# Kernel tuning notes

Measured on AMD Instinct MI355X. Metric: run time of the kernel, lower is better.

## Reference

```python
import jax, jax.numpy as jnp
import numpy as np

N, D, E_LOCAL, E_GLOBAL = 50000, 128, 500000, 600000


def gcn_conv(x, W, b, src, dst, w, n):
    """PyG GCNConv with add_self_loops=True, symmetric normalization.

    deg[i] = sum of incoming edge weights at i + 1 (self-loop weight 1)
    norm_e = deg^-1/2[src] * w_e * deg^-1/2[dst]
    out[i] = sum_e norm_e * (xW)[src_e]  +  deg^-1[i] * (xW)[i]  + b
    """
    xw = x @ W  # [n, out]
    deg = jax.ops.segment_sum(w, dst, num_segments=n) + 1.0
    dinv = jnp.where(deg > 0, jax.lax.rsqrt(deg), 0.0)
    norm = dinv[src] * w * dinv[dst]  # [E]
    agg = jax.ops.segment_sum(norm[:, None] * xw[src], dst, num_segments=n)
    self_loop = (dinv * dinv)[:, None] * xw
    return agg + self_loop + b


def setup_inputs() -> dict:
    key = jax.random.key(0)
    ks = jax.random.split(key, 10)
    activity = jax.random.normal(ks[0], (N, D), dtype=jnp.float32)
    learning = jax.random.normal(ks[1], (N, D), dtype=jnp.float32)
    edge_index = jax.random.randint(ks[2], (2, E_LOCAL), 0, N, dtype=jnp.int32)
    edge_weight = jax.random.uniform(ks[3], (E_LOCAL,), dtype=jnp.float32)
    global_edge_index = jax.random.randint(ks[4], (2, E_GLOBAL), 0, N, dtype=jnp.int32)
    global_edge_weight = jax.random.uniform(ks[5], (E_GLOBAL,), dtype=jnp.float32)
    s = 1.0 / np.sqrt(D)
    W_local = jax.random.uniform(ks[6], (D, D), jnp.float32, -s, s)
    b_local = jnp.zeros((D,), jnp.float32)
    W_global = jax.random.uniform(ks[7], (D, D), jnp.float32, -s, s)
    b_global = jnp.zeros((D,), jnp.float32)
    return {
        "activity": activity, "learning": learning,
        "edge_index": edge_index, "edge_weight": edge_weight,
        "global_edge_index": global_edge_index, "global_edge_weight": global_edge_weight,
        "W_local": W_local, "b_local": b_local,
        "W_global": W_global, "b_global": b_global,
    }


def reference(activity, learning, edge_index, edge_weight,
              global_edge_index, global_edge_weight,
              W_local, b_local, W_global, b_global):
    n = activity.shape[0]
    xa = activity + learning
    # Note: GCNConv1 branches in the original are dead code (outputs overwritten);
    # only GCNConv2 (local and global) affect the output.
    xl = gcn_conv(xa, W_local, b_local, edge_index[0], edge_index[1], edge_weight, n)
    xg = gcn_conv(xa, W_global, b_global, global_edge_index[0], global_edge_index[1], global_edge_weight, n)
    wei = jax.nn.sigmoid(xl + xg)
    return 2.0 * activity * wei + 2.0 * learning * (1.0 - wei)
```

## Files before the change

### kernel.cpp

```cpp
#include <hip/hip_runtime.h>

#define DFEAT 128

typedef __attribute__((ext_vector_type(8))) short short8;
typedef __attribute__((ext_vector_type(4))) float float4v;

__device__ __forceinline__ float bf2f(unsigned int h) {
    union { unsigned int u; float f; } v; v.u = h << 16; return v.f;
}
__device__ __forceinline__ unsigned short f2bf(float f) {
    union { float f; unsigned int u; } v; v.f = f;
    unsigned int u = v.u;
    unsigned int lsb = (u >> 16) & 1u;
    u += 0x7fffu + lsb;
    return (unsigned short)(u >> 16);
}

__global__ __launch_bounds__(256) void zprep_kernel(
    const float* __restrict__ Wl, const float* __restrict__ Wg,
    unsigned short* __restrict__ WT,
    unsigned long long* __restrict__ dc, int n2)
{
    if (blockIdx.x < 128) {
        int idx = blockIdx.x * 256 + threadIdx.x;
        int m = idx >> 14, rem = idx & 16383;
        int k = rem >> 7, c = rem & 127;
        const float* W = m ? Wg : Wl;
        WT[m * 16384 + c * 128 + k] = f2bf(W[k * 128 + c]);
        return;
    }
    int i = (blockIdx.x - 128) * 256 + threadIdx.x;
    if (i < n2) dc[i] = 0ULL;
}

__global__ __launch_bounds__(256) void gemm_hist_kernel(
    const float* __restrict__ A, const float* __restrict__ L,
    const unsigned short* __restrict__ WT,
    unsigned short* __restrict__ xwl, unsigned short* __restrict__ xwg,
    const int* __restrict__ dstL, const float* __restrict__ wL,
    const int* __restrict__ dstG, const float* __restrict__ wG,
    unsigned long long* __restrict__ dc, unsigned short* __restrict__ lp16,
    int El, int Eg, int n, int GB)
{
    if (blockIdx.x >= GB) {
        int e = (blockIdx.x - GB) * 256 + threadIdx.x;
        if (e < El) {
            int t = dstL[e];
            unsigned long long add = (1ULL << 48) | (unsigned long long)(wL[e] * 0x1p40f);
            unsigned long long old = atomicAdd(&dc[t], add);
            lp16[e] = (unsigned short)(old >> 48);
        } else if (e < El + Eg) {
            int e2 = e - El;
            int t = dstG[e2];
            unsigned long long add = (1ULL << 48) | (unsigned long long)(wG[e2] * 0x1p40f);
            unsigned long long old = atomicAdd(&dc[n + t], add);
            lp16[e] = (unsigned short)(old >> 48);
        }
        return;
    }
    const int tid  = threadIdx.x;
    const int wid  = tid >> 6;
    const int lane = tid & 63;
    const int quad = lane >> 4;
    const int cl   = lane & 15;

    int rowa = blockIdx.x * 64 + wid * 16 + cl;
    if (rowa > n - 1) rowa = n - 1;

    const float* Ar = A + (size_t)rowa * DFEAT;
    const float* Lr = L + (size_t)rowa * DFEAT;

    short8 a[4];
    #pragma unroll
    for (int kk = 0; kk < 4; ++kk) {
        const int kb = kk * 32 + quad * 8;
        float4 a0 = *(const float4*)&Ar[kb];
        float4 a1 = *(const float4*)&Ar[kb + 4];
        float4 l0 = *(const float4*)&Lr[kb];
        float4 l1 = *(const float4*)&Lr[kb + 4];
        union { short8 v; unsigned short u[8]; } s;
        s.u[0] = f2bf(a0.x + l0.x); s.u[1] = f2bf(a0.y + l0.y);
        s.u[2] = f2bf(a0.z + l0.z); s.u[3] = f2bf(a0.w + l0.w);
        s.u[4] = f2bf(a1.x + l1.x); s.u[5] = f2bf(a1.y + l1.y);
        s.u[6] = f2bf(a1.z + l1.z); s.u[7] = f2bf(a1.w + l1.w);
        a[kk] = s.v;
    }

    const int rbase = blockIdx.x * 64 + wid * 16 + quad * 4;
    const char* wtb = (const char*)WT + quad * 16;

    #pragma unroll
    for (int m = 0; m < 2; ++m) {
        unsigned short* out = m ? xwg : xwl;
        #pragma unroll
        for (int t = 0; t < 8; ++t) {
            const int col = t * 16 + cl;
            const char* bp = wtb + m * 32768 + col * 256;
            float4v acc = {0.f, 0.f, 0.f, 0.f};
            #pragma unroll
            for (int kk = 0; kk < 4; ++kk) {
                short8 b = *(const short8*)(bp + kk * 64);
                acc = __builtin_amdgcn_mfma_f32_16x16x32_bf16(a[kk], b, acc, 0, 0, 0);
            }
            #pragma unroll
            for (int r = 0; r < 4; ++r) {
                int ro = rbase + r;
                if (ro < n) out[(size_t)ro * DFEAT + col] = f2bf(acc[r]);
            }
        }
    }
}

__global__ __launch_bounds__(256) void scan1_kernel(const unsigned long long* __restrict__ dc,
                                                    int* __restrict__ ptr,
                                                    int* __restrict__ bsum,
                                                    float* __restrict__ dinv, int n)
{
    __shared__ int tmp[256];
    int i = blockIdx.x * 256 + threadIdx.x;
    int v = 0;
    if (i < n) {
        unsigned long long d = dc[i];
        v = (int)(d >> 48);
        dinv[i] = rsqrtf((float)(d & ((1ULL << 48) - 1)) * 0x1p-40f + 1.0f);
    }
    tmp[threadIdx.x] = v;
    __syncthreads();
    for (int off = 1; off < 256; off <<= 1) {
        int t = (threadIdx.x >= off) ? tmp[threadIdx.x - off] : 0;
        __syncthreads();
        tmp[threadIdx.x] += t;
        __syncthreads();
    }
    if (i < n) ptr[i] = tmp[threadIdx.x] - v;
    if (threadIdx.x == 255) bsum[blockIdx.x] = tmp[255];
}

__global__ __launch_bounds__(512) void scan2_kernel(int* __restrict__ bsum, int nb)
{
    __shared__ int tmp[512];
    int i = threadIdx.x;
    int v = (i < nb) ? bsum[i] : 0;
    tmp[i] = v;
    __syncthreads();
    for (int off = 1; off < 512; off <<= 1) {
        int t = (i >= off) ? tmp[i - off] : 0;
        __syncthreads();
        tmp[i] += t;
        __syncthreads();
    }
    if (i < nb) bsum[i] = tmp[i] - v;
}

__global__ __launch_bounds__(256) void edata_write_kernel(
    const int* __restrict__ srcL, const int* __restrict__ dstL, const float* __restrict__ wL,
    const int* __restrict__ srcG, const int* __restrict__ dstG, const float* __restrict__ wG,
    const float* __restrict__ dinv, const int* __restrict__ ptr, const int* __restrict__ bsum,
    const unsigned short* __restrict__ lp16, int2* __restrict__ edata,
    int El, int Eg, int n)
{
    int e = blockIdx.x * 256 + threadIdx.x;
    if (e < El) {
        int s = srcL[e], t = dstL[e];
        float norm = dinv[s] * wL[e] * dinv[t];
        int pos = ptr[t] + bsum[t >> 8] + lp16[e];
        edata[pos] = make_int2(__float_as_int(norm), s);
    } else if (e < El + Eg) {
        int e2 = e - El;
        int s = srcG[e2], t = dstG[e2];
        float norm = dinv[n + s] * wG[e2] * dinv[n + t];
        int tt = n + t;
        int pos = ptr[tt] + bsum[tt >> 8] + lp16[e];
        edata[pos] = make_int2(__float_as_int(norm), s);
    }
}

__global__ __launch_bounds__(256) void gather_kernel(
    const unsigned short* __restrict__ xwl, const unsigned short* __restrict__ xwg,
    const int* __restrict__ ptr, const int* __restrict__ bsum, const int2* __restrict__ edata,
    const float* __restrict__ dinv,
    const float* __restrict__ A, const float* __restrict__ Lr,
    const float* __restrict__ bl, const float* __restrict__ bg,
    float* __restrict__ out, int n, int E)
{
    const int lane = threadIdx.x & 63;
    const int node = blockIdx.x * 4 + (threadIdx.x >> 6);
    if (node >= n) return;
    const int i0l = ptr[node] + bsum[node >> 8];
    const int i1l = ptr[node + 1] + bsum[(node + 1) >> 8];
    const int i0g = ptr[n + node] + bsum[(n + node) >> 8];
    const int i1g = (node == n - 1) ? E : ptr[n + node + 1] + bsum[(n + node + 1) >> 8];
    float dl = dinv[node];     dl *= dl;
    float dg = dinv[n + node]; dg *= dg;
    const int fo = 2 * lane;
    const size_t base = (size_t)node * DFEAT + fo;

    unsigned int psl = *(const unsigned int*)&xwl[base];
    unsigned int psg = *(const unsigned int*)&xwg[base];
    float acc0 = dl * bf2f(psl & 0xffffu) + dg * bf2f(psg & 0xffffu);
    float acc1 = dl * bf2f(psl >> 16)     + dg * bf2f(psg >> 16);

    for (int b0 = i0l; b0 < i1l; b0 += 64) {
        int idx = b0 + lane;
        int2 ed = edata[idx < i1l ? idx : (i1l - 1)];
        float nmv = __int_as_float(ed.x);
        int   sv  = ed.y;
        int mcnt = i1l - b0; if (mcnt > 64) mcnt = 64;
        #pragma unroll 4
        for (int jj = 0; jj < mcnt; ++jj) {
            float nm = __shfl(nmv, jj);
            int   s  = __shfl(sv, jj);
            unsigned int pk = *(const unsigned int*)&xwl[(size_t)s * DFEAT + fo];
            acc0 += nm * bf2f(pk & 0xffffu);
            acc1 += nm * bf2f(pk >> 16);
        }
    }
    for (int b0 = i0g; b0 < i1g; b0 += 64) {
        int idx = b0 + lane;
        int2 ed = edata[idx < i1g ? idx : (i1g - 1)];
        float nmv = __int_as_float(ed.x);
        int   sv  = ed.y;
        int mcnt = i1g - b0; if (mcnt > 64) mcnt = 64;
        #pragma unroll 4
        for (int jj = 0; jj < mcnt; ++jj) {
            float nm = __shfl(nmv, jj);
            int   s  = __shfl(sv, jj);
            unsigned int pk = *(const unsigned int*)&xwg[(size_t)s * DFEAT + fo];
            acc0 += nm * bf2f(pk & 0xffffu);
            acc1 += nm * bf2f(pk >> 16);
        }
    }

    float2 b1 = *(const float2*)&bl[fo];
    float2 b2 = *(const float2*)&bg[fo];
    float2 a2 = *(const float2*)&A[base];
    float2 l2 = *(const float2*)&Lr[base];
    float v0 = acc0 + b1.x + b2.x;
    float v1 = acc1 + b1.y + b2.y;
    float w0 = 1.0f / (1.0f + __expf(-v0));
    float w1 = 1.0f / (1.0f + __expf(-v1));
    float o0 = 2.0f * (a2.x * w0 + l2.x * (1.0f - w0));
    float o1 = 2.0f * (a2.y * w1 + l2.y * (1.0f - w1));
    *(float2*)&out[base] = make_float2(o0, o1);
}

extern "C" void kernel_launch(void* const* d_in, const int* in_sizes, int n_in,
                              void* d_out, int out_size, void* d_ws, size_t ws_size,
                              hipStream_t stream)
{
    const float* activity = (const float*)d_in[0];
    const float* learning = (const float*)d_in[1];
    const int*   ei  = (const int*)d_in[2];
    const float* ew  = (const float*)d_in[3];
    const int*   gei = (const int*)d_in[4];
    const float* gew = (const float*)d_in[5];
    const float* Wl  = (const float*)d_in[6];
    const float* bl  = (const float*)d_in[7];
    const float* Wg  = (const float*)d_in[8];
    const float* bg  = (const float*)d_in[9];

    const int n  = in_sizes[0] / DFEAT;
    const int El = in_sizes[3];
    const int Eg = in_sizes[5];
    const int n2 = 2 * n;
    const int E  = El + Eg;

    char* ws = (char*)d_ws;
    const size_t xwBytes = (size_t)n * DFEAT * 2;
    unsigned short* xwl = (unsigned short*)ws;
    unsigned short* xwg = (unsigned short*)(ws + xwBytes);
    unsigned long long* dc = (unsigned long long*)(ws + 2 * xwBytes);
    float* dinv = (float*)(ws + 2 * xwBytes + (size_t)n2 * 8);
    int*   ptr  = (int*)(ws + 2 * xwBytes + (size_t)n2 * 12);
    int*   bsum = (int*)(ws + 2 * xwBytes + (size_t)n2 * 16);
    unsigned short* WT = (unsigned short*)(ws + 2 * xwBytes + (size_t)n2 * 16 + 2048);
    int2* edata = (int2*)(ws + 2 * xwBytes + (size_t)n2 * 16 + 2048 + 65536);
    unsigned short* lp16 = (unsigned short*)(ws + 2 * xwBytes + (size_t)n2 * 16 + 2048 + 65536
                                             + (size_t)E * 8);

    const int scanBlocks = (n2 + 255) / 256;
    const int GB = (n + 63) / 64;
    const int HB = (E + 255) / 256;

    zprep_kernel<<<dim3(128 + scanBlocks), dim3(256), 0, stream>>>(Wl, Wg, WT, dc, n2);

    gemm_hist_kernel<<<dim3(GB + HB), dim3(256), 0, stream>>>(
        activity, learning, WT, xwl, xwg,
        ei + El, ew, gei + Eg, gew, dc, lp16, El, Eg, n, GB);

    scan1_kernel<<<dim3(scanBlocks), dim3(256), 0, stream>>>(dc, ptr, bsum, dinv, n2);
    scan2_kernel<<<dim3(1), dim3(512), 0, stream>>>(bsum, scanBlocks);

    edata_write_kernel<<<dim3(HB), dim3(256), 0, stream>>>(
        ei, ei + El, ew, gei, gei + Eg, gew, dinv, ptr, bsum, lp16, edata, El, Eg, n);

    gather_kernel<<<dim3((n + 3) / 4), dim3(256), 0, stream>>>(
        xwl, xwg, ptr, bsum, edata, dinv, activity, learning, bl, bg, (float*)d_out, n, E);
}
```

Before: 277.3 us.

## Split wavefront into four edge groups with 16-byte feature loads in gather

```diff
diff --git a/kernel.cpp b/kernel.cpp
--- a/kernel.cpp
+++ b/kernel.cpp
@@ -14,6 +14,12 @@
     unsigned int lsb = (u >> 16) & 1u;
     u += 0x7fffu + lsb;
     return (unsigned short)(u >> 16);
+}
+__device__ __forceinline__ float blo(unsigned int u) {
+    union { unsigned int x; float f; } v; v.x = u << 16; return v.f;
+}
+__device__ __forceinline__ float bhi(unsigned int u) {
+    union { unsigned int x; float f; } v; v.x = u & 0xffff0000u; return v.f;
 }
 
 __global__ __launch_bounds__(256) void zprep_kernel(
@@ -184,35 +190,43 @@
     float* __restrict__ out, int n, int E)
 {
     const int lane = threadIdx.x & 63;
+    const int grp  = lane >> 4;
+    const int fl   = lane & 15;
     const int node = blockIdx.x * 4 + (threadIdx.x >> 6);
     if (node >= n) return;
+
     const int i0l = ptr[node] + bsum[node >> 8];
     const int i1l = ptr[node + 1] + bsum[(node + 1) >> 8];
     const int i0g = ptr[n + node] + bsum[(n + node) >> 8];
     const int i1g = (node == n - 1) ? E : ptr[n + node + 1] + bsum[(n + node + 1) >> 8];
     float dl = dinv[node];     dl *= dl;
     float dg = dinv[n + node]; dg *= dg;
-    const int fo = 2 * lane;
-    const size_t base = (size_t)node * DFEAT + fo;
-
-    unsigned int psl = *(const unsigned int*)&xwl[base];
-    unsigned int psg = *(const unsigned int*)&xwg[base];
-    float acc0 = dl * bf2f(psl & 0xffffu) + dg * bf2f(psg & 0xffffu);
-    float acc1 = dl * bf2f(psl >> 16)     + dg * bf2f(psg >> 16);
+
+    const int fo = fl * 8;
+    const size_t nbase = (size_t)node * DFEAT + fo;
+    const uint4 svl = *(const uint4*)&xwl[nbase];
+    const uint4 svg = *(const uint4*)&xwg[nbase];
+
+    float acc[8] = {0.f, 0.f, 0.f, 0.f, 0.f, 0.f, 0.f, 0.f};
 
     for (int b0 = i0l; b0 < i1l; b0 += 64) {
         int idx = b0 + lane;
         int2 ed = edata[idx < i1l ? idx : (i1l - 1)];
         float nmv = __int_as_float(ed.x);
         int   sv  = ed.y;
-        int mcnt = i1l - b0; if (mcnt > 64) mcnt = 64;
-        #pragma unroll 4
-        for (int jj = 0; jj < mcnt; ++jj) {
-            float nm = __shfl(nmv, jj);
-            int   s  = __shfl(sv, jj);
-            unsigned int pk = *(const unsigned int*)&xwl[(size_t)s * DFEAT + fo];
-            acc0 += nm * bf2f(pk & 0xffffu);
-            acc1 += nm * bf2f(pk >> 16);
+        int cnt = i1l - b0; if (cnt > 64) cnt = 64;
+        int iters = (cnt + 3) >> 2;
+        #pragma unroll 2
+        for (int jj = 0; jj < iters; ++jj) {
+            int sl = 4 * jj + grp;
+            float nm = __shfl(nmv, sl);
+            int   s  = __shfl(sv,  sl);
+            if (sl >= cnt) nm = 0.f;
+            uint4 pk = *(const uint4*)&xwl[(size_t)s * DFEAT + fo];
+            acc[0] += nm * blo(pk.x); acc[1] += nm * bhi(pk.x);
+            acc[2] += nm * blo(pk.y); acc[3] += nm * bhi(pk.y);
+            acc[4] += nm * blo(pk.z); acc[5] += nm * bhi(pk.z);
+            acc[6] += nm * blo(pk.w); acc[7] += nm * bhi(pk.w);
         }
     }
     for (int b0 = i0g; b0 < i1g; b0 += 64) {
@@ -220,28 +234,57 @@
         int2 ed = edata[idx < i1g ? idx : (i1g - 1)];
         float nmv = __int_as_float(ed.x);
         int   sv  = ed.y;
-        int mcnt = i1g - b0; if (mcnt > 64) mcnt = 64;
-        #pragma unroll 4
-        for (int jj = 0; jj < mcnt; ++jj) {
-            float nm = __shfl(nmv, jj);
-            int   s  = __shfl(sv, jj);
-            unsigned int pk = *(const unsigned int*)&xwg[(size_t)s * DFEAT + fo];
-            acc0 += nm * bf2f(pk & 0xffffu);
-            acc1 += nm * bf2f(pk >> 16);
+        int cnt = i1g - b0; if (cnt > 64) cnt = 64;
+        int iters = (cnt + 3) >> 2;
+        #pragma unroll 2
+        for (int jj = 0; jj < iters; ++jj) {
+            int sl = 4 * jj + grp;
+            float nm = __shfl(nmv, sl);
+            int   s  = __shfl(sv,  sl);
+            if (sl >= cnt) nm = 0.f;
+            uint4 pk = *(const uint4*)&xwg[(size_t)s * DFEAT + fo];
+            acc[0] += nm * blo(pk.x); acc[1] += nm * bhi(pk.x);
+            acc[2] += nm * blo(pk.y); acc[3] += nm * bhi(pk.y);
+            acc[4] += nm * blo(pk.z); acc[5] += nm * bhi(pk.z);
+            acc[6] += nm * blo(pk.w); acc[7] += nm * bhi(pk.w);
         }
     }
 
-    float2 b1 = *(const float2*)&bl[fo];
-    float2 b2 = *(const float2*)&bg[fo];
-    float2 a2 = *(const float2*)&A[base];
-    float2 l2 = *(const float2*)&Lr[base];
-    float v0 = acc0 + b1.x + b2.x;
-    float v1 = acc1 + b1.y + b2.y;
+    #pragma unroll
+    for (int j = 0; j < 8; ++j) {
+        acc[j] += __shfl_xor(acc[j], 16);
+        acc[j] += __shfl_xor(acc[j], 32);
+    }
+
+    acc[0] += dl * blo(svl.x) + dg * blo(svg.x);
+    acc[1] += dl * bhi(svl.x) + dg * bhi(svg.x);
+    acc[2] += dl * blo(svl.y) + dg * blo(svg.y);
+    acc[3] += dl * bhi(svl.y) + dg * bhi(svg.y);
+    acc[4] += dl * blo(svl.z) + dg * blo(svg.z);
+    acc[5] += dl * bhi(svl.z) + dg * bhi(svg.z);
+    acc[6] += dl * blo(svl.w) + dg * blo(svg.w);
+    acc[7] += dl * bhi(svl.w) + dg * bhi(svg.w);
+
+    float s0a = (grp & 1) ? acc[2] : acc[0];
+    float s1a = (grp & 1) ? acc[3] : acc[1];
+    float s0b = (grp & 1) ? acc[6] : acc[4];
+    float s1b = (grp & 1) ? acc[7] : acc[5];
+    float v0 = (grp & 2) ? s0b : s0a;
+    float v1 = (grp & 2) ? s1b : s1a;
+
+    const int f0 = fo + grp * 2;
+    const size_t obase = (size_t)node * DFEAT + f0;
+    float2 b1 = *(const float2*)&bl[f0];
+    float2 b2 = *(const float2*)&bg[f0];
+    float2 a2 = *(const float2*)&A[obase];
+    float2 l2 = *(const float2*)&Lr[obase];
+    v0 += b1.x + b2.x;
+    v1 += b1.y + b2.y;
     float w0 = 1.0f / (1.0f + __expf(-v0));
     float w1 = 1.0f / (1.0f + __expf(-v1));
     float o0 = 2.0f * (a2.x * w0 + l2.x * (1.0f - w0));
     float o1 = 2.0f * (a2.y * w1 + l2.y * (1.0f - w1));
-    *(float2*)&out[base] = make_float2(o0, o1);
+    *(float2*)&out[obase] = make_float2(o0, o1);
 }
 
 extern "C" void kernel_launch(void* const* d_in, const int* in_sizes, int n_in,
```

New measurement: 254.6 us. 1.09x faster.
